# Optimization experiments

Hardware: AMD Instinct MI355X
Metric: run time of the kernel (lower is better)

## Reference

```python
import jax, jax.numpy as jnp
import numpy as np

D_MODEL = 1024
D_STATE = 16
EXPAND = 2
D_INNER = EXPAND * D_MODEL          # 2048
DT_RANK = D_MODEL // 16             # 64
BATCH = 2
LENGTH = 2048


def setup_inputs() -> dict:
    key = jax.random.key(0)
    ks = jax.random.split(key, 10)
    s = 0.02
    x = jax.random.normal(ks[0], (BATCH, LENGTH, D_MODEL), jnp.float32)
    W_in = jax.random.normal(ks[1], (D_MODEL, 2 * D_INNER), jnp.float32) * s
    b_in = jnp.zeros((2 * D_INNER,), jnp.float32)
    W_x = jax.random.normal(ks[2], (D_INNER, DT_RANK + 2 * D_STATE), jnp.float32) * s
    b_x = jnp.zeros((DT_RANK + 2 * D_STATE,), jnp.float32)
    W_dt = jax.random.normal(ks[3], (DT_RANK, D_INNER), jnp.float32) * s
    b_dt = jnp.zeros((D_INNER,), jnp.float32)
    # A = arange(1..d_state) repeated per channel; A_log = log(A)
    A_log = jnp.log(jnp.tile(jnp.arange(1, D_STATE + 1, dtype=jnp.float32), (D_INNER, 1)))
    D = jnp.ones((D_INNER,), jnp.float32)
    W_out = jax.random.normal(ks[4], (D_INNER, D_MODEL), jnp.float32) * s
    b_out = jnp.zeros((D_MODEL,), jnp.float32)
    return dict(x=x, W_in=W_in, b_in=b_in, W_x=W_x, b_x=b_x,
                W_dt=W_dt, b_dt=b_dt, A_log=A_log, D=D,
                W_out=W_out, b_out=b_out)


def reference(x, W_in, b_in, W_x, b_x, W_dt, b_dt, A_log, D, W_out, b_out):
    b, l, _ = x.shape
    # input projection -> gate split
    xz = x @ W_in + b_in                       # [b, l, 2*d_inner]
    x_inner, z = jnp.split(xz, 2, axis=-1)     # each [b, l, d_inner]

    # depthwise causal conv, kernel = ones(3)/3, left pad 2 (trailing mean of 3)
    xp = jnp.pad(x_inner, ((0, 0), (2, 0), (0, 0)))
    x_conv = (xp[:, 0:l] + xp[:, 1:l + 1] + xp[:, 2:l + 2]) / 3.0
    x_conv = jax.nn.silu(x_conv)

    # SSM parameters per timestep
    x_dbl = x_conv @ W_x + b_x                 # [b, l, dt_rank + 2*d_state]
    dt, Bm, Cm = jnp.split(x_dbl, [DT_RANK, DT_RANK + D_STATE], axis=-1)
    dt = jax.nn.softplus(dt @ W_dt + b_dt)     # [b, l, d_inner]
    A = -jnp.exp(A_log)                        # [d_inner, d_state]

    def step(h, inp):
        dt_t, B_t, C_t, x_t = inp              # [b,d], [b,n], [b,n], [b,d]
        dA = jnp.exp(A[None] * dt_t[..., None])            # [b, d, n]
        h = dA * h + (dt_t * x_t)[..., None] * B_t[:, None, :]
        y = jnp.einsum('bdn,bn->bd', h, C_t)
        return h, y

    h0 = jnp.zeros((b, D_INNER, D_STATE), x.dtype)
    seq = (dt.transpose(1, 0, 2), Bm.transpose(1, 0, 2),
           Cm.transpose(1, 0, 2), x_conv.transpose(1, 0, 2))
    _, ys = jax.lax.scan(step, h0, seq)        # ys: [l, b, d_inner]
    y = ys.transpose(1, 0, 2) + x_conv * D

    out = (y * jax.nn.silu(z)) @ W_out + b_out
    return out
```

## Files before the change

kernel.cpp:

```cpp
#include <hip/hip_runtime.h>
#include <hip/hip_bf16.h>

typedef __attribute__((ext_vector_type(8))) short short8;
typedef __attribute__((ext_vector_type(4))) float f32x4;
typedef __attribute__((ext_vector_type(4))) float float4v;

#define NCHUNK 16
#define CT 128

static __device__ __forceinline__ unsigned short f2bf(float f) {
    union { float f; unsigned u; } v; v.f = f;
    unsigned r = v.u + 0x7fff + ((v.u >> 16) & 1);
    return (unsigned short)(r >> 16);
}

static __device__ __forceinline__ void gld16(const unsigned short* g, unsigned short* l) {
    __builtin_amdgcn_global_load_lds(
        (const __attribute__((address_space(1))) void*)g,
        (__attribute__((address_space(3))) void*)l, 16, 0, 0);
}

__global__ __launch_bounds__(256) void cast_bf16(
    const float* __restrict__ in, unsigned short* __restrict__ out, int n8)
{
    int i = blockIdx.x * 256 + threadIdx.x;
    if (i >= n8) return;
    const float4v v0 = *reinterpret_cast<const float4v*>(in + (size_t)i * 8);
    const float4v v1 = *reinterpret_cast<const float4v*>(in + (size_t)i * 8 + 4);
    short8 t;
    t[0] = (short)f2bf(v0[0]); t[1] = (short)f2bf(v0[1]);
    t[2] = (short)f2bf(v0[2]); t[3] = (short)f2bf(v0[3]);
    t[4] = (short)f2bf(v1[0]); t[5] = (short)f2bf(v1[1]);
    t[6] = (short)f2bf(v1[2]); t[7] = (short)f2bf(v1[3]);
    *reinterpret_cast<short8*>(out + (size_t)i * 8) = t;
}

__global__ __launch_bounds__(256) void transpose_bf16(
    const float* __restrict__ in, unsigned short* __restrict__ out, int R, int Cc)
{
    __shared__ float tile[32][33];
    int c0 = blockIdx.x * 32, r0 = blockIdx.y * 32;
    int tx = threadIdx.x, ty = threadIdx.y;
#pragma unroll
    for (int i = 0; i < 32; i += 8) {
        int r = r0 + ty + i, c = c0 + tx;
        tile[ty + i][tx] = (r < R && c < Cc) ? in[(size_t)r * Cc + c] : 0.f;
    }
    __syncthreads();
#pragma unroll
    for (int i = 0; i < 32; i += 8) {
        int c = c0 + ty + i, r = r0 + tx;
        if (c < Cc && r < R) out[(size_t)c * R + r] = f2bf(tile[tx][ty + i]);
    }
}

template <int ACT, bool AUX>
__global__ __launch_bounds__(256) void gemm_bf(
    const unsigned short* __restrict__ A, int lda,
    const unsigned short* __restrict__ Bt, int ldb,
    const float* __restrict__ bias,
    float* __restrict__ C, int ldc,
    unsigned short* __restrict__ Cbf, int ldcbf, int ncbf,
    int N, int K)
{
    __shared__ __align__(16) unsigned short As[128 * 32];
    __shared__ __align__(16) unsigned short Bs[128 * 32];

    const int tid  = threadIdx.x;
    const int lane = tid & 63;
    const int wave = tid >> 6;
    const int g    = lane >> 4;
    const int r16  = lane & 15;
    const int wr   = (wave >> 1) * 64;
    const int wc   = (wave & 1) * 64;
    const int rowBase = blockIdx.y * 128;
    const int colBase = blockIdx.x * 128;

    const int e0 = tid * 8;
    const int e1 = (256 + tid) * 8;
    const int r0 = e0 >> 5, c0 = e0 & 31;
    const int r1 = e1 >> 5, c1 = e1 & 31;
    const unsigned short* a0 = A + (size_t)(rowBase + r0) * lda + c0;
    const unsigned short* a1 = A + (size_t)(rowBase + r1) * lda + c1;
    const unsigned short* b0 = Bt + (size_t)(colBase + r0) * ldb + c0;
    const unsigned short* b1 = Bt + (size_t)(colBase + r1) * ldb + c1;

    f32x4 acc[4][4] = {};

    for (int k0 = 0; k0 < K; k0 += 32) {
        gld16(a0 + k0, As + e0);
        gld16(a1 + k0, As + e1);
        gld16(b0 + k0, Bs + e0);
        gld16(b1 + k0, Bs + e1);
        __syncthreads();

        short8 af[4], bfr[4];
#pragma unroll
        for (int m = 0; m < 4; ++m)
            af[m] = *reinterpret_cast<const short8*>(&As[(wr + m * 16 + r16) * 32 + g * 8]);
#pragma unroll
        for (int n = 0; n < 4; ++n)
            bfr[n] = *reinterpret_cast<const short8*>(&Bs[(wc + n * 16 + r16) * 32 + g * 8]);
#pragma unroll
        for (int m = 0; m < 4; ++m)
#pragma unroll
            for (int n = 0; n < 4; ++n)
                acc[m][n] = __builtin_amdgcn_mfma_f32_16x16x32_bf16(
                    af[m], bfr[n], acc[m][n], 0, 0, 0);
        __syncthreads();
    }

#pragma unroll
    for (int m = 0; m < 4; ++m) {
#pragma unroll
        for (int v = 0; v < 4; ++v) {
            int gr = rowBase + wr + m * 16 + g * 4 + v;
#pragma unroll
            for (int n = 0; n < 4; ++n) {
                int gc = colBase + wc + n * 16 + r16;
                if (gc >= N) continue;
                float val = acc[m][n][v] + bias[gc];
                if (ACT == 1) val = (val > 20.f) ? val : log1pf(expf(val));
                C[(size_t)gr * ldc + gc] = val;
                if (AUX && gc < ncbf)
                    Cbf[(size_t)gr * ldcbf + gc] = f2bf(val);
            }
        }
    }
}

template <int ACT>
__global__ __launch_bounds__(256) void gemm_mfma(
    const float* __restrict__ A, int lda,
    const unsigned short* __restrict__ Bt, int ldb,
    const float* __restrict__ bias,
    float* __restrict__ C, int ldc,
    int M, int N, int K)
{
    __shared__ unsigned short As[128 * 32];
    __shared__ unsigned short Bs[128 * 32];

    const int tid  = threadIdx.x;
    const int lane = tid & 63;
    const int wave = tid >> 6;
    const int g    = lane >> 4;
    const int r16  = lane & 15;
    const int wr   = (wave >> 1) * 64;
    const int wc   = (wave & 1) * 64;
    const int rowBase = blockIdx.y * 128;
    const int colBase = blockIdx.x * 128;

    f32x4 acc[4][4] = {};

    for (int k0 = 0; k0 < K; k0 += 32) {
#pragma unroll
        for (int c = 0; c < 2; ++c) {
            int chunk = c * 256 + tid;
            int r = chunk >> 2, slot = chunk & 3;
            int gr = rowBase + r;
            short8 t = {};
            if (gr < M) {
                const float* src = A + (size_t)gr * lda + k0 + slot * 8;
                float4v v0 = *reinterpret_cast<const float4v*>(src);
                float4v v1 = *reinterpret_cast<const float4v*>(src + 4);
                t[0] = (short)f2bf(v0[0]); t[1] = (short)f2bf(v0[1]);
                t[2] = (short)f2bf(v0[2]); t[3] = (short)f2bf(v0[3]);
                t[4] = (short)f2bf(v1[0]); t[5] = (short)f2bf(v1[1]);
                t[6] = (short)f2bf(v1[2]); t[7] = (short)f2bf(v1[3]);
            }
            int sslot = slot ^ (r & 3);
            *reinterpret_cast<short8*>(&As[r * 32 + sslot * 8]) = t;
        }
#pragma unroll
        for (int c = 0; c < 2; ++c) {
            int chunk = c * 256 + tid;
            int r = chunk >> 2, slot = chunk & 3;
            int gn = colBase + r;
            short8 t = {};
            if (gn < N)
                t = *reinterpret_cast<const short8*>(Bt + (size_t)gn * ldb + k0 + slot * 8);
            int sslot = slot ^ (r & 3);
            *reinterpret_cast<short8*>(&Bs[r * 32 + sslot * 8]) = t;
        }
        __syncthreads();

        short8 af[4], bfr[4];
#pragma unroll
        for (int m = 0; m < 4; ++m) {
            int r = wr + m * 16 + r16;
            af[m] = *reinterpret_cast<const short8*>(&As[r * 32 + (g ^ (r & 3)) * 8]);
        }
#pragma unroll
        for (int n = 0; n < 4; ++n) {
            int r = wc + n * 16 + r16;
            bfr[n] = *reinterpret_cast<const short8*>(&Bs[r * 32 + (g ^ (r & 3)) * 8]);
        }
#pragma unroll
        for (int m = 0; m < 4; ++m)
#pragma unroll
            for (int n = 0; n < 4; ++n)
                acc[m][n] = __builtin_amdgcn_mfma_f32_16x16x32_bf16(
                    af[m], bfr[n], acc[m][n], 0, 0, 0);
        __syncthreads();
    }

#pragma unroll
    for (int m = 0; m < 4; ++m) {
#pragma unroll
        for (int v = 0; v < 4; ++v) {
            int gr = rowBase + wr + m * 16 + g * 4 + v;
            if (gr >= M) continue;
#pragma unroll
            for (int n = 0; n < 4; ++n) {
                int gc = colBase + wc + n * 16 + r16;
                if (gc >= N) continue;
                float val = acc[m][n][v] + bias[gc];
                if (ACT == 1) val = (val > 20.f) ? val : log1pf(expf(val));
                C[(size_t)gr * ldc + gc] = val;
            }
        }
    }
}

template <bool BF>
__global__ __launch_bounds__(256) void conv_silu(
    const float* __restrict__ xz, float* __restrict__ xconv,
    unsigned short* __restrict__ xconv_bf)
{
    int idx = blockIdx.x * blockDim.x + threadIdx.x;
    if (idx >= 4096 * 2048) return;
    int d = idx & 2047;
    int row = idx >> 11;
    int l = row & 2047;

    float s = xz[(size_t)row * 4096 + d];
    if (l >= 1) s += xz[(size_t)(row - 1) * 4096 + d];
    if (l >= 2) s += xz[(size_t)(row - 2) * 4096 + d];
    s *= (1.f / 3.f);
    float sv = s / (1.f + __expf(-s));
    xconv[idx] = sv;
    if (BF) xconv_bf[idx] = f2bf(sv);
}

__global__ __launch_bounds__(256) void scan_passA(
    const float* __restrict__ dt,
    const float* __restrict__ xdbl,
    const float* __restrict__ xconv,
    const float* __restrict__ A_log,
    float* __restrict__ Pc,
    float* __restrict__ Sc)
{
    __shared__ float sBC[CT][32];
    const int tid  = threadIdx.x;
    const int bid  = blockIdx.x;
    const int dg   = bid & 31;
    const int c    = (bid >> 5) & 15;
    const int b    = bid >> 9;
    const int lane = tid & 63;
    const int wave = tid >> 6;
    const int chi  = lane & 15;
    const int ng   = lane >> 4;
    const int d    = dg * 64 + wave * 16 + chi;
    const size_t rowBase = (size_t)b * 2048 + (size_t)c * CT;

    for (int i = tid; i < CT * 8; i += 256) {
        int tt = i >> 3, q = i & 7;
        *reinterpret_cast<float4v*>(&sBC[tt][q * 4]) =
            *reinterpret_cast<const float4v*>(&xdbl[(rowBase + tt) * 96 + 64 + q * 4]);
    }
    __syncthreads();

    float4v Aval, h = {}, P = {1.f, 1.f, 1.f, 1.f};
#pragma unroll
    for (int j = 0; j < 4; ++j) Aval[j] = -expf(A_log[d * 16 + ng * 4 + j]);

    const float* pdt = dt + rowBase * 2048 + d;
    const float* px  = xconv + rowBase * 2048 + d;
    float dt_c = *pdt, x_c = *px;
    for (int t = 0; t < CT; ++t) {
        float dt_n = 0.f, x_n = 0.f;
        if (t + 1 < CT) { dt_n = pdt[2048]; x_n = px[2048]; }
        pdt += 2048; px += 2048;

        float4v Bv = *reinterpret_cast<const float4v*>(&sBC[t][ng * 4]);
        float u = dt_c * x_c;
#pragma unroll
        for (int j = 0; j < 4; ++j) {
            float dA = __expf(Aval[j] * dt_c);
            P[j] *= dA;
            h[j] = dA * h[j] + u * Bv[j];
        }
        dt_c = dt_n; x_c = x_n;
    }
    size_t o = (((size_t)(b * NCHUNK + c)) * 2048 + d) * 16 + ng * 4;
    *reinterpret_cast<float4v*>(&Pc[o]) = P;
    *reinterpret_cast<float4v*>(&Sc[o]) = h;
}

template <int WMODE>
__global__ __launch_bounds__(256) void scan_passC2(
    const float* __restrict__ dt,
    const float* __restrict__ xdbl,
    const float* __restrict__ xz,
    float* __restrict__ xconv,
    const float* __restrict__ A_log,
    const float* __restrict__ Dp,
    const float* __restrict__ Pc,
    const float* __restrict__ Sc,
    unsigned short* __restrict__ gated_bf)
{
    __shared__ float sBC[CT][32];
    const int tid  = threadIdx.x;
    const int bid  = blockIdx.x;
    const int dg   = bid & 31;
    const int c    = (bid >> 5) & 15;
    const int b    = bid >> 9;
    const int lane = tid & 63;
    const int wave = tid >> 6;
    const int chi  = lane & 15;
    const int ng   = lane >> 4;
    const int d    = dg * 64 + wave * 16 + chi;
    const size_t rowBase = (size_t)b * 2048 + (size_t)c * CT;

    for (int i = tid; i < CT * 8; i += 256) {
        int tt = i >> 3, q = i & 7;
        *reinterpret_cast<float4v*>(&sBC[tt][q * 4]) =
            *reinterpret_cast<const float4v*>(&xdbl[(rowBase + tt) * 96 + 64 + q * 4]);
    }
    __syncthreads();

    float4v Aval, h = {};
#pragma unroll
    for (int j = 0; j < 4; ++j) Aval[j] = -expf(A_log[d * 16 + ng * 4 + j]);
    const float Dval = Dp[d];

    for (int cp = 0; cp < c; ++cp) {
        size_t o = (((size_t)(b * NCHUNK + cp)) * 2048 + d) * 16 + ng * 4;
        float4v Pv = *reinterpret_cast<const float4v*>(&Pc[o]);
        float4v Sv = *reinterpret_cast<const float4v*>(&Sc[o]);
#pragma unroll
        for (int j = 0; j < 4; ++j) h[j] = Pv[j] * h[j] + Sv[j];
    }

    const float* pdt = dt + rowBase * 2048 + d;
    const float* px  = xconv + rowBase * 2048 + d;
    const float* pz  = xz + rowBase * 4096 + 2048 + d;
    float* pw        = xconv + rowBase * 2048 + d;
    unsigned short* pwb = gated_bf + rowBase * 2048 + d;
    float dt_c = *pdt, x_c = *px;

    for (int t = 0; t < CT; ++t) {
        float dt_n = 0.f, x_n = 0.f;
        if (t + 1 < CT) { dt_n = pdt[2048]; x_n = px[2048]; }
        pdt += 2048; px += 2048;

        float4v Bv = *reinterpret_cast<const float4v*>(&sBC[t][ng * 4]);
        float4v Cv = *reinterpret_cast<const float4v*>(&sBC[t][16 + ng * 4]);
        float u = dt_c * x_c;
        float p = 0.f;
#pragma unroll
        for (int j = 0; j < 4; ++j) {
            float dA = __expf(Aval[j] * dt_c);
            h[j] = dA * h[j] + u * Bv[j];
            p += h[j] * Cv[j];
        }
        p += __shfl_xor(p, 16);
        p += __shfl_xor(p, 32);

        if (ng == 0) {
            float y = p + x_c * Dval;
            float zv = *pz;
            float sz = zv / (1.f + __expf(-zv));
            float gv = y * sz;
            if (WMODE == 0) *pw = gv;
            else            *pwb = f2bf(gv);
        }
        pz += 4096; pw += 2048; pwb += 2048;
        dt_c = dt_n; x_c = x_n;
    }
}

__global__ __launch_bounds__(256) void scan_kernel(
    const float* __restrict__ dt, const float* __restrict__ xdbl,
    const float* __restrict__ xz, float* __restrict__ xconv,
    const float* __restrict__ A_log, const float* __restrict__ Dp)
{
    const int L = 2048, DI = 2048;
    const int n = threadIdx.x & 15;
    const int chi = threadIdx.x >> 4;
    const int b = blockIdx.x / 128;
    const int d = (blockIdx.x % 128) * 16 + chi;

    const float Aval = -expf(A_log[d * 16 + n]);
    const float Dval = Dp[d];
    float h = 0.f;
    const size_t rowBase = (size_t)b * L;

    float dt_c = dt[rowBase * DI + d];
    float x_c  = xconv[rowBase * DI + d];
    float B_c  = xdbl[rowBase * 96 + 64 + n];
    float C_c  = xdbl[rowBase * 96 + 80 + n];

    for (int t = 0; t < L; ++t) {
        size_t row = rowBase + t;
        float dt_n = 0.f, x_n = 0.f, B_n = 0.f, C_n = 0.f;
        if (t + 1 < L) {
            size_t rn = row + 1;
            dt_n = dt[rn * DI + d];
            x_n  = xconv[rn * DI + d];
            B_n  = xdbl[rn * 96 + 64 + n];
            C_n  = xdbl[rn * 96 + 80 + n];
        }
        float dA = __expf(Aval * dt_c);
        h = dA * h + (dt_c * x_c) * B_c;
        float p = h * C_c;
        p += __shfl_xor(p, 1, 16);
        p += __shfl_xor(p, 2, 16);
        p += __shfl_xor(p, 4, 16);
        p += __shfl_xor(p, 8, 16);
        if (n == 0) {
            float y = p + x_c * Dval;
            float zv = xz[row * 4096 + 2048 + d];
            float sz = zv / (1.f + __expf(-zv));
            xconv[row * DI + d] = y * sz;
        }
        dt_c = dt_n; x_c = x_n; B_c = B_n; C_c = C_n;
    }
}

extern "C" void kernel_launch(void* const* d_in, const int* in_sizes, int n_in,
                              void* d_out, int out_size, void* d_ws, size_t ws_size,
                              hipStream_t stream)
{
    const float* x     = (const float*)d_in[0];
    const float* W_in  = (const float*)d_in[1];
    const float* b_in  = (const float*)d_in[2];
    const float* W_x   = (const float*)d_in[3];
    const float* b_x   = (const float*)d_in[4];
    const float* W_dt  = (const float*)d_in[5];
    const float* b_dt  = (const float*)d_in[6];
    const float* A_log = (const float*)d_in[7];
    const float* Dp    = (const float*)d_in[8];
    const float* W_out = (const float*)d_in[9];
    const float* b_out = (const float*)d_in[10];
    float* out = (float*)d_out;

    float* ws    = (float*)d_ws;
    float* xz    = ws;
    float* xconv = xz + 16777216;
    float* xdbl  = xconv + 8388608;
    float* dtbuf = xdbl + 393216;
    float* Pc    = dtbuf + 8388608;
    float* Sc    = Pc + 1048576;

    const size_t base_f32 = 16777216 + 8388608 + 393216 + 8388608;
    const size_t wshorts  = 4096 * 1024 + 96 * 2048 + 2048 * 64 + 1024 * 2048;
    const size_t bfshorts = 4096 * 1024 + 8388608 + 4096 * 64 + 8388608;
    const size_t needed_bf   = (base_f32 + 2 * 1048576) * 4 + (wshorts + bfshorts) * 2;
    const size_t needed_full = (base_f32 + 2 * 1048576) * 4 + wshorts * 2;
    const size_t needed_fall = base_f32 * 4 + wshorts * 2;

    const int tier = (ws_size >= needed_bf) ? 1 : (ws_size >= needed_full) ? 2
                   : (ws_size >= needed_fall) ? 3 : 0;
    if (tier == 0) return;

    unsigned short* wbuf = (tier == 3) ? (unsigned short*)Pc
                                       : (unsigned short*)(Sc + 1048576);
    unsigned short* WinT  = wbuf;
    unsigned short* WxT   = WinT  + 4096 * 1024;
    unsigned short* WdtT  = WxT   + 96 * 2048;
    unsigned short* WoutT = WdtT  + 2048 * 64;
    unsigned short* x_bf     = WoutT + 1024 * 2048;
    unsigned short* xconv_bf = x_bf + 4096 * 1024;
    unsigned short* xdbl_bf  = xconv_bf + 8388608;
    unsigned short* gated_bf = xdbl_bf + 4096 * 64;

    dim3 tblk(32, 8);
    transpose_bf16<<<dim3(128, 32), tblk, 0, stream>>>(W_in, WinT, 1024, 4096);
    transpose_bf16<<<dim3(3, 64),   tblk, 0, stream>>>(W_x,  WxT,  2048, 96);
    transpose_bf16<<<dim3(64, 2),   tblk, 0, stream>>>(W_dt, WdtT, 64, 2048);
    transpose_bf16<<<dim3(32, 64),  tblk, 0, stream>>>(W_out,WoutT,2048, 1024);

    dim3 blk(256);

    if (tier == 1) {
        cast_bf16<<<2048, blk, 0, stream>>>(x, x_bf, 4096 * 1024 / 8);

        gemm_bf<0, false><<<dim3(32, 32), blk, 0, stream>>>(
            x_bf, 1024, WinT, 1024, b_in, xz, 4096, nullptr, 0, 0, 4096, 1024);

        conv_silu<true><<<(4096 * 2048 + 255) / 256, blk, 0, stream>>>(
            xz, xconv, xconv_bf);

        gemm_bf<0, true><<<dim3(1, 32), blk, 0, stream>>>(
            xconv_bf, 2048, WxT, 2048, b_x, xdbl, 96, xdbl_bf, 64, 64, 96, 2048);

        gemm_bf<1, false><<<dim3(16, 32), blk, 0, stream>>>(
            xdbl_bf, 64, WdtT, 64, b_dt, dtbuf, 2048, nullptr, 0, 0, 2048, 64);

        scan_passA<<<1024, blk, 0, stream>>>(dtbuf, xdbl, xconv, A_log, Pc, Sc);
        scan_passC2<1><<<1024, blk, 0, stream>>>(
            dtbuf, xdbl, xz, xconv, A_log, Dp, Pc, Sc, gated_bf);

        gemm_bf<0, false><<<dim3(8, 32), blk, 0, stream>>>(
            gated_bf, 2048, WoutT, 2048, b_out, out, 1024, nullptr, 0, 0, 1024, 2048);
    } else {
        gemm_mfma<0><<<dim3(32, 32), blk, 0, stream>>>(
            x, 1024, WinT, 1024, b_in, xz, 4096, 4096, 4096, 1024);
        conv_silu<false><<<(4096 * 2048 + 255) / 256, blk, 0, stream>>>(
            xz, xconv, nullptr);
        gemm_mfma<0><<<dim3(1, 32), blk, 0, stream>>>(
            xconv, 2048, WxT, 2048, b_x, xdbl, 96, 4096, 96, 2048);
        gemm_mfma<1><<<dim3(16, 32), blk, 0, stream>>>(
            xdbl, 96, WdtT, 64, b_dt, dtbuf, 2048, 4096, 2048, 64);
        if (tier == 2) {
            scan_passA<<<1024, blk, 0, stream>>>(dtbuf, xdbl, xconv, A_log, Pc, Sc);
            scan_passC2<0><<<1024, blk, 0, stream>>>(
                dtbuf, xdbl, xz, xconv, A_log, Dp, Pc, Sc, (unsigned short*)xconv);
        } else {
            scan_kernel<<<256, blk, 0, stream>>>(dtbuf, xdbl, xz, xconv, A_log, Dp);
        }
        gemm_mfma<0><<<dim3(8, 32), blk, 0, stream>>>(
            xconv, 2048, WoutT, 2048, b_out, out, 1024, 4096, 1024, 2048);
    }
}
```

Before: 493.6 us.

## Halve scan chunk length and add separate inter-chunk prefix pass

Doubles the number of scan chunks (64 timesteps each) so pass A and pass C launch twice as many blocks. A new pass B kernel computes each chunk's carried-in state with one sequential combine over chunks, replacing the quadratic per-block recombination of all earlier chunks inside pass C. The bf16 gated output now reuses the xconv_bf buffer, and the workspace tiers are simplified, dropping the fp32 chunked-scan fallback. The cost is one extra small kernel launch and a larger Pc/Sc state buffer.

```diff
diff --git a/kernel.cpp b/kernel.cpp
--- a/kernel.cpp
+++ b/kernel.cpp
@@ -5,8 +5,8 @@
 typedef __attribute__((ext_vector_type(4))) float f32x4;
 typedef __attribute__((ext_vector_type(4))) float float4v;
 
-#define NCHUNK 16
-#define CT 128
+#define NCHUNK 32
+#define CT 64
 
 static __device__ __forceinline__ unsigned short f2bf(float f) {
     union { float f; unsigned u; } v; v.f = f;
@@ -242,6 +242,7 @@
     if (BF) xconv_bf[idx] = f2bf(sv);
 }
 
+
 __global__ __launch_bounds__(256) void scan_passA(
     const float* __restrict__ dt,
     const float* __restrict__ xdbl,
@@ -254,8 +255,8 @@
     const int tid  = threadIdx.x;
     const int bid  = blockIdx.x;
     const int dg   = bid & 31;
-    const int c    = (bid >> 5) & 15;
-    const int b    = bid >> 9;
+    const int c    = (bid >> 5) & 31;
+    const int b    = bid >> 10;
     const int lane = tid & 63;
     const int wave = tid >> 6;
     const int chi  = lane & 15;
@@ -297,24 +298,41 @@
     *reinterpret_cast<float4v*>(&Sc[o]) = h;
 }
 
-template <int WMODE>
+__global__ __launch_bounds__(256) void scan_passB(
+    float* __restrict__ Pc, const float* __restrict__ Sc)
+{
+    int idx = blockIdx.x * 256 + threadIdx.x;
+    int ng  = idx & 3;
+    int d   = (idx >> 2) & 2047;
+    int b   = idx >> 13;
+    float4v h = {};
+#pragma unroll
+    for (int c = 0; c < NCHUNK; ++c) {
+        size_t o = (((size_t)(b * NCHUNK + c)) * 2048 + d) * 16 + ng * 4;
+        float4v Pv = *reinterpret_cast<const float4v*>(&Pc[o]);
+        float4v Sv = *reinterpret_cast<const float4v*>(&Sc[o]);
+        *reinterpret_cast<float4v*>(&Pc[o]) = h;
+#pragma unroll
+        for (int j = 0; j < 4; ++j) h[j] = Pv[j] * h[j] + Sv[j];
+    }
+}
+
 __global__ __launch_bounds__(256) void scan_passC2(
     const float* __restrict__ dt,
     const float* __restrict__ xdbl,
     const float* __restrict__ xz,
-    float* __restrict__ xconv,
+    const float* __restrict__ xconv,
     const float* __restrict__ A_log,
     const float* __restrict__ Dp,
     const float* __restrict__ Pc,
-    const float* __restrict__ Sc,
     unsigned short* __restrict__ gated_bf)
 {
     __shared__ float sBC[CT][32];
     const int tid  = threadIdx.x;
     const int bid  = blockIdx.x;
     const int dg   = bid & 31;
-    const int c    = (bid >> 5) & 15;
-    const int b    = bid >> 9;
+    const int c    = (bid >> 5) & 31;
+    const int b    = bid >> 10;
     const int lane = tid & 63;
     const int wave = tid >> 6;
     const int chi  = lane & 15;
@@ -329,23 +347,17 @@
     }
     __syncthreads();
 
-    float4v Aval, h = {};
+    float4v Aval;
 #pragma unroll
     for (int j = 0; j < 4; ++j) Aval[j] = -expf(A_log[d * 16 + ng * 4 + j]);
     const float Dval = Dp[d];
 
-    for (int cp = 0; cp < c; ++cp) {
-        size_t o = (((size_t)(b * NCHUNK + cp)) * 2048 + d) * 16 + ng * 4;
-        float4v Pv = *reinterpret_cast<const float4v*>(&Pc[o]);
-        float4v Sv = *reinterpret_cast<const float4v*>(&Sc[o]);
-#pragma unroll
-        for (int j = 0; j < 4; ++j) h[j] = Pv[j] * h[j] + Sv[j];
-    }
+    float4v h = *reinterpret_cast<const float4v*>(
+        &Pc[(((size_t)(b * NCHUNK + c)) * 2048 + d) * 16 + ng * 4]);
 
     const float* pdt = dt + rowBase * 2048 + d;
     const float* px  = xconv + rowBase * 2048 + d;
     const float* pz  = xz + rowBase * 4096 + 2048 + d;
-    float* pw        = xconv + rowBase * 2048 + d;
     unsigned short* pwb = gated_bf + rowBase * 2048 + d;
     float dt_c = *pdt, x_c = *px;
 
@@ -371,11 +383,9 @@
             float y = p + x_c * Dval;
             float zv = *pz;
             float sz = zv / (1.f + __expf(-zv));
-            float gv = y * sz;
-            if (WMODE == 0) *pw = gv;
-            else            *pwb = f2bf(gv);
-        }
-        pz += 4096; pw += 2048; pwb += 2048;
+            *pwb = f2bf(y * sz);
+        }
+        pz += 4096; pwb += 2048;
         dt_c = dt_n; x_c = x_n;
     }
 }
@@ -451,21 +461,19 @@
     float* xdbl  = xconv + 8388608;
     float* dtbuf = xdbl + 393216;
     float* Pc    = dtbuf + 8388608;
-    float* Sc    = Pc + 1048576;
+    float* Sc    = Pc + 2097152;
 
     const size_t base_f32 = 16777216 + 8388608 + 393216 + 8388608;
     const size_t wshorts  = 4096 * 1024 + 96 * 2048 + 2048 * 64 + 1024 * 2048;
-    const size_t bfshorts = 4096 * 1024 + 8388608 + 4096 * 64 + 8388608;
-    const size_t needed_bf   = (base_f32 + 2 * 1048576) * 4 + (wshorts + bfshorts) * 2;
-    const size_t needed_full = (base_f32 + 2 * 1048576) * 4 + wshorts * 2;
-    const size_t needed_fall = base_f32 * 4 + wshorts * 2;
-
-    const int tier = (ws_size >= needed_bf) ? 1 : (ws_size >= needed_full) ? 2
-                   : (ws_size >= needed_fall) ? 3 : 0;
+    const size_t bfshorts = 4096 * 1024 + 8388608 + 4096 * 64;
+    const size_t needed_t1 = (base_f32 + 2 * 2097152) * 4 + (wshorts + bfshorts) * 2;
+    const size_t needed_t2 = base_f32 * 4 + wshorts * 2;
+
+    const int tier = (ws_size >= needed_t1) ? 1 : (ws_size >= needed_t2) ? 2 : 0;
     if (tier == 0) return;
 
-    unsigned short* wbuf = (tier == 3) ? (unsigned short*)Pc
-                                       : (unsigned short*)(Sc + 1048576);
+    unsigned short* wbuf = (tier == 1) ? (unsigned short*)(Sc + 2097152)
+                                       : (unsigned short*)Pc;
     unsigned short* WinT  = wbuf;
     unsigned short* WxT   = WinT  + 4096 * 1024;
     unsigned short* WdtT  = WxT   + 96 * 2048;
@@ -473,7 +481,7 @@
     unsigned short* x_bf     = WoutT + 1024 * 2048;
     unsigned short* xconv_bf = x_bf + 4096 * 1024;
     unsigned short* xdbl_bf  = xconv_bf + 8388608;
-    unsigned short* gated_bf = xdbl_bf + 4096 * 64;
+    unsigned short* gated_bf = xconv_bf;
 
     dim3 tblk(32, 8);
     transpose_bf16<<<dim3(128, 32), tblk, 0, stream>>>(W_in, WinT, 1024, 4096);
@@ -498,9 +506,10 @@
         gemm_bf<1, false><<<dim3(16, 32), blk, 0, stream>>>(
             xdbl_bf, 64, WdtT, 64, b_dt, dtbuf, 2048, nullptr, 0, 0, 2048, 64);
 
-        scan_passA<<<1024, blk, 0, stream>>>(dtbuf, xdbl, xconv, A_log, Pc, Sc);
-        scan_passC2<1><<<1024, blk, 0, stream>>>(
-            dtbuf, xdbl, xz, xconv, A_log, Dp, Pc, Sc, gated_bf);
+        scan_passA<<<2048, blk, 0, stream>>>(dtbuf, xdbl, xconv, A_log, Pc, Sc);
+        scan_passB<<<64, blk, 0, stream>>>(Pc, Sc);
+        scan_passC2<<<2048, blk, 0, stream>>>(
+            dtbuf, xdbl, xz, xconv, A_log, Dp, Pc, gated_bf);
 
         gemm_bf<0, false><<<dim3(8, 32), blk, 0, stream>>>(
             gated_bf, 2048, WoutT, 2048, b_out, out, 1024, nullptr, 0, 0, 1024, 2048);
@@ -513,13 +522,7 @@
             xconv, 2048, WxT, 2048, b_x, xdbl, 96, 4096, 96, 2048);
         gemm_mfma<1><<<dim3(16, 32), blk, 0, stream>>>(
             xdbl, 96, WdtT, 64, b_dt, dtbuf, 2048, 4096, 2048, 64);
-        if (tier == 2) {
-            scan_passA<<<1024, blk, 0, stream>>>(dtbuf, xdbl, xconv, A_log, Pc, Sc);
-            scan_passC2<0><<<1024, blk, 0, stream>>>(
-                dtbuf, xdbl, xz, xconv, A_log, Dp, Pc, Sc, (unsigned short*)xconv);
-        } else {
-            scan_kernel<<<256, blk, 0, stream>>>(dtbuf, xdbl, xz, xconv, A_log, Dp);
-        }
+        scan_kernel<<<256, blk, 0, stream>>>(dtbuf, xdbl, xz, xconv, A_log, Dp);
         gemm_mfma<0><<<dim3(8, 32), blk, 0, stream>>>(
             xconv, 2048, WoutT, 2048, b_out, out, 1024, 4096, 1024, 2048);
     }
```

Result: faster. 457.9 us (-7.2%).
